# Kernel tuning notes

Hardware: AMD Instinct MI355X
Metric: run time of the kernel (lower is better)

The kernel has to match this reference:

```python
import jax, jax.numpy as jnp
import numpy as np
from jax import lax

NUM_TAGS = 126
T = NUM_TAGS + 2          # tag_size = 128
B, S = 256, 512
START, STOP = T - 3, T - 2
NEG = -10000.0


def setup_inputs() -> dict:
    key = jax.random.key(0)
    k1, k2, k3 = jax.random.split(key, 3)
    feats = jax.random.normal(k1, (B, S, T), jnp.float32)
    # learned transition matrix with the module's init masking pattern
    trans = jax.random.normal(k2, (T, T), jnp.float32)
    trans = trans.at[:, START].set(NEG).at[STOP, :].set(NEG)
    trans = trans.at[:, 0].set(NEG).at[0, :].set(NEG)
    # prefix masks with varying valid lengths in [S/2, S]
    lengths = jax.random.randint(k3, (B,), S // 2, S + 1)
    mask = jnp.arange(S)[None, :] < lengths[:, None]
    return {"feats": feats, "mask": mask, "transitions": trans}


def reference(feats, mask, transitions):
    # Viterbi decode (module.forward returns (None, decode_idx)).
    Bn, Sn, Tn = feats.shape
    start, stop = Tn - 3, Tn - 2
    emit = jnp.transpose(feats, (1, 0, 2))            # (S, B, T)
    m = jnp.transpose(mask.astype(jnp.int32))         # (S, B)
    lengths = mask.astype(jnp.int32).sum(axis=1)      # (B,)

    part0 = emit[0] + transitions[start][None, :]     # (B, T)

    def step(part, inp):
        e_t, m_t = inp
        # scores[t, b, i, j] = feats[t, b, j] + transitions[i, j]
        cur = part[:, :, None] + transitions[None, :, :] + e_t[:, None, :]  # (B, from, to)
        new_part = cur.max(axis=1)                                          # (B, T)
        bp = jnp.argmax(cur, axis=1).astype(jnp.int32)                      # (B, T)
        bp = jnp.where(m_t[:, None] > 0, bp, 0)
        return new_part, (new_part, bp)

    _, (hist, bps) = lax.scan(step, part0, (emit[1:], m[1:]))
    part_hist = jnp.concatenate([part0[None], hist], axis=0)                # (S, B, T)
    back_points = jnp.concatenate(
        [bps, jnp.zeros((1, Bn, Tn), jnp.int32)], axis=0)                   # (S, B, T)

    bidx = jnp.arange(Bn)
    last_pos = lengths - 1                                                  # (B,)
    last_partition = part_hist[last_pos, bidx]                              # (B, T)
    last_bp = jnp.argmax(last_partition[:, :, None] + transitions[None], axis=1)
    pointer = last_bp[:, stop].astype(jnp.int32)                            # (B,)

    # overwrite back_points at the last valid position with the final pointer
    bp_bt = jnp.transpose(back_points, (1, 0, 2))                           # (B, S, T)
    bp_bt = bp_bt.at[bidx, last_pos].set(
        jnp.broadcast_to(pointer[:, None], (Bn, Tn)))
    back_points = jnp.transpose(bp_bt, (1, 0, 2))                           # (S, B, T)

    def trace(ptr, bp_t):
        new_ptr = jnp.take_along_axis(bp_t, ptr[:, None], axis=1)[:, 0]
        return new_ptr, new_ptr

    _, rev = lax.scan(trace, pointer, back_points[:-1], reverse=True)       # (S-1, B)
    decode = jnp.concatenate([rev, pointer[None]], axis=0)                  # (S, B)
    return jnp.transpose(decode)                                            # (B, S)
```

## Files before the change

### kernel.cpp

```cpp
#include <hip/hip_runtime.h>
#include <cstdint>
#include <cstddef>

constexpr int T_ = 128;
constexpr int S_ = 512;
constexpr int B_ = 256;
constexpr int START_ = T_ - 3;
constexpr int STOP_  = T_ - 2;
constexpr float NEGINF_ = -3.402823466e38f;

__global__ __launch_bounds__(256) void viterbi_forward(
    const float* __restrict__ feats,
    const float* __restrict__ trans,
    float* __restrict__ ph)
{
  const int b   = blockIdx.x;
  const int tid = threadIdx.x;
  const int j   = tid & (T_ - 1);
  const int h   = tid >> 7;

  __shared__ alignas(16) float part[T_];
  __shared__ float partial[2][T_];

  float tc[64];
  #pragma unroll
  for (int ii = 0; ii < 64; ++ii)
    tc[ii] = trans[(h * 64 + ii) * T_ + j];

  const float* fb = feats + (size_t)b * S_ * T_;

  float p0 = fb[j] + trans[START_ * T_ + j];
  if (h == 0) {
    part[j] = p0;
    ph[(size_t)b * T_ + j] = p0;
  }
  float e_next = fb[T_ + j];
  __syncthreads();

  for (int t = 1; t < S_; ++t) {
    float e_cur = e_next;
    if (t + 1 < S_) e_next = fb[(size_t)(t + 1) * T_ + j];

    const float4* p4 = (const float4*)part;
    float ma = NEGINF_, mb = NEGINF_;
    #pragma unroll
    for (int q = 0; q < 16; q += 2) {
      float4 pa = p4[h * 16 + q];
      float a0 = pa.x + tc[4 * q + 0];
      float a1 = pa.y + tc[4 * q + 1];
      float a2 = pa.z + tc[4 * q + 2];
      float a3 = pa.w + tc[4 * q + 3];
      ma = fmaxf(ma, fmaxf(fmaxf(a0, a1), fmaxf(a2, a3)));
      float4 pb = p4[h * 16 + q + 1];
      float b0 = pb.x + tc[4 * q + 4];
      float b1 = pb.y + tc[4 * q + 5];
      float b2 = pb.z + tc[4 * q + 6];
      float b3 = pb.w + tc[4 * q + 7];
      mb = fmaxf(mb, fmaxf(fmaxf(b0, b1), fmaxf(b2, b3)));
    }
    partial[h][j] = fmaxf(ma, mb);
    __syncthreads();
    if (h == 0) {
      float np = fmaxf(partial[0][j], partial[1][j]) + e_cur;
      part[j] = np;
      ph[((size_t)t * B_ + b) * T_ + j] = np;
    }
    __syncthreads();
  }
}

constexpr int CH_ = 8;

__global__ __launch_bounds__(64) void viterbi_trace(
    const float* __restrict__ feats,
    const void*  __restrict__ mask,
    const float* __restrict__ trans,
    const float* __restrict__ ph,
    int* __restrict__ out)
{
  const int b    = blockIdx.x;
  const int lane = threadIdx.x;

  __shared__ float transT[T_ * 129];

  #pragma unroll 4
  for (int g = lane; g < T_ * T_; g += 64) {
    int i  = g >> 7;
    int jj = g & (T_ - 1);
    transT[jj * 129 + i] = trans[g];
  }
  __syncthreads();

  int len = 0;
  {
    const int w0 = *(const int*)mask;
    if (w0 == 0x01010101) {
      const unsigned char* m = (const unsigned char*)mask + (size_t)b * S_;
      for (int s = lane; s < S_; s += 64) len += (m[s] != 0);
    } else if (w0 == 0x3F800000) {
      const float* m = (const float*)mask + (size_t)b * S_;
      for (int s = lane; s < S_; s += 64) len += (m[s] != 0.0f);
    } else {
      const int* m = (const int*)mask + (size_t)b * S_;
      for (int s = lane; s < S_; s += 64) len += (m[s] != 0);
    }
    #pragma unroll
    for (int o = 32; o > 0; o >>= 1) len += __shfl_xor(len, o);
  }
  const int lp = len - 1;

  const float* lastrow = ph + ((size_t)lp * B_ + b) * T_;
  float v0 = lastrow[lane]      + transT[STOP_ * 129 + lane];
  float v1 = lastrow[lane + 64] + transT[STOP_ * 129 + 64 + lane];
  float mx = fmaxf(v0, v1);
  #pragma unroll
  for (int o = 32; o > 0; o >>= 1) mx = fmaxf(mx, __shfl_xor(mx, o));
  unsigned long long g0 = __ballot(v0 == mx);
  unsigned long long g1 = __ballot(v1 == mx);
  int pointer = g0 ? (__ffsll(g0) - 1) : (64 + __ffsll(g1) - 1);

  int ptr = pointer;
  if (lane == 0) out[b * S_ + (S_ - 1)] = pointer;

  const float* fb = feats + (size_t)b * S_ * T_;

  float Aph[CH_][2], Apn[CH_][2], Afe[CH_][2];
  float Bph[CH_][2], Bpn[CH_][2], Bfe[CH_][2];

  auto issue = [&](float (&P)[CH_][2], float (&N)[CH_][2], float (&F)[CH_][2],
                   int k0) {
    #pragma unroll
    for (int s = 0; s < CH_; ++s) {
      int k = k0 - s;
      if (k < 0) k = 0;
      const float* rp = ph + ((size_t)k       * B_ + b) * T_;
      const float* rn = ph + ((size_t)(k + 1) * B_ + b) * T_;
      const float* rf = fb + (size_t)(k + 1) * T_;
      P[s][0] = rp[lane];      P[s][1] = rp[lane + 64];
      N[s][0] = rn[lane];      N[s][1] = rn[lane + 64];
      F[s][0] = rf[lane];      F[s][1] = rf[lane + 64];
    }
  };

  auto process = [&](float (&P)[CH_][2], float (&N)[CH_][2], float (&F)[CH_][2],
                     int k0) {
    #pragma unroll
    for (int s = 0; s < CH_; ++s) {
      const int kk = k0 - s;
      if (kk >= 0) {
        int val;
        if (kk > lp) {
          val = 0;
        } else if (kk == lp) {
          ptr = pointer;
          val = pointer;
        } else {
          float tr0 = transT[ptr * 129 + lane];
          float tr1 = transT[ptr * 129 + 64 + lane];
          const int pl = ptr & 63;
          float e  = __shfl((ptr < 64) ? F[s][0] : F[s][1], pl);
          float tg = __shfl((ptr < 64) ? N[s][0] : N[s][1], pl);
          float c0 = (P[s][0] + tr0) + e;
          float c1 = (P[s][1] + tr1) + e;
          unsigned long long m0 = __ballot(c0 == tg);
          unsigned long long m1 = __ballot(c1 == tg);
          ptr = m0 ? (__ffsll(m0) - 1) : (64 + __ffsll(m1) - 1);
          val = ptr;
        }
        if (lane == 0) out[b * S_ + kk] = val;
      }
    }
  };

  issue(Aph, Apn, Afe, S_ - 2);
  for (int k0 = S_ - 2; k0 >= 0; k0 -= 2 * CH_) {
    issue(Bph, Bpn, Bfe, k0 - CH_);
    process(Aph, Apn, Afe, k0);
    issue(Aph, Apn, Afe, k0 - 2 * CH_);
    process(Bph, Bpn, Bfe, k0 - CH_);
  }
}

extern "C" void kernel_launch(void* const* d_in, const int* in_sizes, int n_in,
                              void* d_out, int out_size, void* d_ws, size_t ws_size,
                              hipStream_t stream) {
  const float* feats = (const float*)d_in[0];
  const void*  mask  = d_in[1];
  const float* trans = (const float*)d_in[2];
  float* ph = (float*)d_ws;
  int*   out = (int*)d_out;

  viterbi_forward<<<dim3(B_), dim3(256), 0, stream>>>(feats, trans, ph);
  viterbi_trace  <<<dim3(B_), dim3(64),  0, stream>>>(feats, mask, trans, ph, out);
}
```

Measured before the change: 473.9 us.

## Use shuffle reduction and double-buffered LDS in forward; batch chains in traceback

In the forward kernel the two halves of each column now sit in adjacent lanes, so the partial maxima are combined with a shuffle instead of a shared-memory round trip. The partition vector is double-buffered, which removes one of the two barriers per step, and the barrier becomes a raw waitcnt plus s_barrier. The traceback kernel now interleaves four batch chains per wave, reusing the previous step's partition row as the target value and keeping a rolling prefetch window of depth four. The aim is shorter per-step latency on both serial recurrences, at the cost of a quarter as many trace blocks and more register pressure.

```diff
diff --git a/kernel.cpp b/kernel.cpp
--- a/kernel.cpp
+++ b/kernel.cpp
@@ -9,6 +9,10 @@
 constexpr int STOP_  = T_ - 2;
 constexpr float NEGINF_ = -3.402823466e38f;
 
+__device__ __forceinline__ void lds_barrier() {
+  asm volatile("s_waitcnt lgkmcnt(0)\n\ts_barrier" ::: "memory");
+}
+
 __global__ __launch_bounds__(256) void viterbi_forward(
     const float* __restrict__ feats,
     const float* __restrict__ trans,
@@ -16,11 +20,10 @@
 {
   const int b   = blockIdx.x;
   const int tid = threadIdx.x;
-  const int j   = tid & (T_ - 1);
-  const int h   = tid >> 7;
+  const int j   = tid >> 1;
+  const int h   = tid & 1;
 
-  __shared__ alignas(16) float part[T_];
-  __shared__ float partial[2][T_];
+  __shared__ alignas(16) float part[2][T_];
 
   float tc[64];
   #pragma unroll
@@ -31,7 +34,7 @@
 
   float p0 = fb[j] + trans[START_ * T_ + j];
   if (h == 0) {
-    part[j] = p0;
+    part[0][j] = p0;
     ph[(size_t)b * T_ + j] = p0;
   }
   float e_next = fb[T_ + j];
@@ -41,35 +44,35 @@
     float e_cur = e_next;
     if (t + 1 < S_) e_next = fb[(size_t)(t + 1) * T_ + j];
 
-    const float4* p4 = (const float4*)part;
-    float ma = NEGINF_, mb = NEGINF_;
+    const float4* p4 = (const float4*)part[(t - 1) & 1];
+    float m0 = NEGINF_, m1 = NEGINF_, m2 = NEGINF_, m3 = NEGINF_;
     #pragma unroll
-    for (int q = 0; q < 16; q += 2) {
-      float4 pa = p4[h * 16 + q];
-      float a0 = pa.x + tc[4 * q + 0];
-      float a1 = pa.y + tc[4 * q + 1];
-      float a2 = pa.z + tc[4 * q + 2];
-      float a3 = pa.w + tc[4 * q + 3];
-      ma = fmaxf(ma, fmaxf(fmaxf(a0, a1), fmaxf(a2, a3)));
-      float4 pb = p4[h * 16 + q + 1];
-      float b0 = pb.x + tc[4 * q + 4];
-      float b1 = pb.y + tc[4 * q + 5];
-      float b2 = pb.z + tc[4 * q + 6];
-      float b3 = pb.w + tc[4 * q + 7];
-      mb = fmaxf(mb, fmaxf(fmaxf(b0, b1), fmaxf(b2, b3)));
+    for (int q = 0; q < 16; q += 4) {
+      float4 a0 = p4[h * 16 + q + 0];
+      float4 a1 = p4[h * 16 + q + 1];
+      float4 a2 = p4[h * 16 + q + 2];
+      float4 a3 = p4[h * 16 + q + 3];
+      m0 = fmaxf(m0, fmaxf(fmaxf(a0.x + tc[4*q+ 0], a0.y + tc[4*q+ 1]),
+                           fmaxf(a0.z + tc[4*q+ 2], a0.w + tc[4*q+ 3])));
+      m1 = fmaxf(m1, fmaxf(fmaxf(a1.x + tc[4*q+ 4], a1.y + tc[4*q+ 5]),
+                           fmaxf(a1.z + tc[4*q+ 6], a1.w + tc[4*q+ 7])));
+      m2 = fmaxf(m2, fmaxf(fmaxf(a2.x + tc[4*q+ 8], a2.y + tc[4*q+ 9]),
+                           fmaxf(a2.z + tc[4*q+10], a2.w + tc[4*q+11])));
+      m3 = fmaxf(m3, fmaxf(fmaxf(a3.x + tc[4*q+12], a3.y + tc[4*q+13]),
+                           fmaxf(a3.z + tc[4*q+14], a3.w + tc[4*q+15])));
     }
-    partial[h][j] = fmaxf(ma, mb);
-    __syncthreads();
-    if (h == 0) {
-      float np = fmaxf(partial[0][j], partial[1][j]) + e_cur;
-      part[j] = np;
-      ph[((size_t)t * B_ + b) * T_ + j] = np;
-    }
-    __syncthreads();
+    float m = fmaxf(fmaxf(m0, m1), fmaxf(m2, m3));
+    m = fmaxf(m, __shfl_xor(m, 1));
+    float np = m + e_cur;
+    if (h == 0) part[t & 1][j] = np;
+    lds_barrier();
+    if (h == 0) ph[((size_t)t * B_ + b) * T_ + j] = np;
   }
 }
 
-constexpr int CH_ = 8;
+constexpr int NC_ = 4;
+constexpr int D_  = 4;
+constexpr int TS_ = 130;
 
 __global__ __launch_bounds__(64) void viterbi_trace(
     const float* __restrict__ feats,
@@ -78,22 +81,27 @@
     const float* __restrict__ ph,
     int* __restrict__ out)
 {
-  const int b    = blockIdx.x;
   const int lane = threadIdx.x;
+  const int b0   = blockIdx.x * NC_;
 
-  __shared__ float transT[T_ * 129];
-
+  __shared__ alignas(16) float transT[T_ * TS_];
   #pragma unroll 4
   for (int g = lane; g < T_ * T_; g += 64) {
-    int i  = g >> 7;
-    int jj = g & (T_ - 1);
-    transT[jj * 129 + i] = trans[g];
+    int i = g >> 7, jj = g & (T_ - 1);
+    transT[jj * TS_ + i] = trans[g];
   }
   __syncthreads();
 
-  int len = 0;
-  {
-    const int w0 = *(const int*)mask;
+  const int w0 = *(const int*)mask;
+
+  int    lp[NC_], ptrc[NC_], pointer[NC_];
+  float  tg[NC_], e[NC_];
+  float2 P[NC_][D_], F[NC_][D_];
+
+  #pragma unroll
+  for (int c = 0; c < NC_; ++c) {
+    const int b = b0 + c;
+    int len = 0;
     if (w0 == 0x01010101) {
       const unsigned char* m = (const unsigned char*)mask + (size_t)b * S_;
       for (int s = lane; s < S_; s += 64) len += (m[s] != 0);
@@ -106,78 +114,68 @@
     }
     #pragma unroll
     for (int o = 32; o > 0; o >>= 1) len += __shfl_xor(len, o);
+    lp[c] = len - 1;
+
+    float2 L = ((const float2*)(ph + ((size_t)lp[c] * B_ + b) * T_))[lane];
+    float v0 = L.x + transT[STOP_ * TS_ + 2 * lane];
+    float v1 = L.y + transT[STOP_ * TS_ + 2 * lane + 1];
+    float mx = fmaxf(v0, v1);
+    #pragma unroll
+    for (int o = 32; o > 0; o >>= 1) mx = fmaxf(mx, __shfl_xor(mx, o));
+    unsigned long long m0 = __ballot(v0 == mx);
+    unsigned long long m1 = __ballot(v1 == mx);
+    int p0 = m0 ? 2 * (__ffsll(m0) - 1)     : (1 << 30);
+    int p1 = m1 ? 2 * (__ffsll(m1) - 1) + 1 : (1 << 30);
+    int p  = min(p0, p1);
+    pointer[c] = p;
+    ptrc[c]    = p;
+    if (lane == 0) out[b * S_ + (S_ - 1)] = p;
+
+    tg[c] = __shfl((p & 1) ? L.y : L.x, p >> 1);
+    float2 FL = ((const float2*)(feats + ((size_t)b * S_ + lp[c]) * T_))[lane];
+    e[c] = __shfl((p & 1) ? FL.y : FL.x, p >> 1);
+
+    #pragma unroll
+    for (int d = 0; d < D_; ++d) {
+      int kr = S_ - 2 - d; if (kr < 0) kr = 0;
+      P[c][d] = ((const float2*)(ph    + ((size_t)kr * B_ + b) * T_))[lane];
+      F[c][d] = ((const float2*)(feats + ((size_t)b * S_ + kr) * T_))[lane];
+    }
   }
-  const int lp = len - 1;
 
-  const float* lastrow = ph + ((size_t)lp * B_ + b) * T_;
-  float v0 = lastrow[lane]      + transT[STOP_ * 129 + lane];
-  float v1 = lastrow[lane + 64] + transT[STOP_ * 129 + 64 + lane];
-  float mx = fmaxf(v0, v1);
-  #pragma unroll
-  for (int o = 32; o > 0; o >>= 1) mx = fmaxf(mx, __shfl_xor(mx, o));
-  unsigned long long g0 = __ballot(v0 == mx);
-  unsigned long long g1 = __ballot(v1 == mx);
-  int pointer = g0 ? (__ffsll(g0) - 1) : (64 + __ffsll(g1) - 1);
+  for (int k = S_ - 2; k >= 0; --k) {
+    #pragma unroll
+    for (int c = 0; c < NC_; ++c) {
+      const int b = b0 + c;
+      int val;
+      if (k > lp[c]) {
+        val = 0;
+      } else if (k == lp[c]) {
+        ptrc[c] = pointer[c];
+        val = pointer[c];
+      } else {
+        const float* tr = transT + ptrc[c] * TS_ + 2 * lane;
+        float cx = (P[c][0].x + tr[0]) + e[c];
+        float cy = (P[c][0].y + tr[1]) + e[c];
+        unsigned long long q0 = __ballot(cx == tg[c]);
+        unsigned long long q1 = __ballot(cy == tg[c]);
+        int a0 = q0 ? 2 * (__ffsll(q0) - 1)     : (1 << 30);
+        int a1 = q1 ? 2 * (__ffsll(q1) - 1) + 1 : (1 << 30);
+        ptrc[c] = min(a0, a1);
+        val = ptrc[c];
+      }
+      if (lane == 0) out[b * S_ + k] = val;
 
-  int ptr = pointer;
-  if (lane == 0) out[b * S_ + (S_ - 1)] = pointer;
+      int p = ptrc[c], pl = p >> 1;
+      tg[c] = __shfl((p & 1) ? P[c][0].y : P[c][0].x, pl);
+      e[c]  = __shfl((p & 1) ? F[c][0].y : F[c][0].x, pl);
 
-  const float* fb = feats + (size_t)b * S_ * T_;
-
-  float Aph[CH_][2], Apn[CH_][2], Afe[CH_][2];
-  float Bph[CH_][2], Bpn[CH_][2], Bfe[CH_][2];
-
-  auto issue = [&](float (&P)[CH_][2], float (&N)[CH_][2], float (&F)[CH_][2],
-                   int k0) {
-    #pragma unroll
-    for (int s = 0; s < CH_; ++s) {
-      int k = k0 - s;
-      if (k < 0) k = 0;
-      const float* rp = ph + ((size_t)k       * B_ + b) * T_;
-      const float* rn = ph + ((size_t)(k + 1) * B_ + b) * T_;
-      const float* rf = fb + (size_t)(k + 1) * T_;
-      P[s][0] = rp[lane];      P[s][1] = rp[lane + 64];
-      N[s][0] = rn[lane];      N[s][1] = rn[lane + 64];
-      F[s][0] = rf[lane];      F[s][1] = rf[lane + 64];
+      #pragma unroll
+      for (int d = 0; d < D_ - 1; ++d) { P[c][d] = P[c][d + 1]; F[c][d] = F[c][d + 1]; }
+      int kr = k - D_; if (kr < 0) kr = 0;
+      P[c][D_ - 1] = ((const float2*)(ph    + ((size_t)kr * B_ + b) * T_))[lane];
+      F[c][D_ - 1] = ((const float2*)(feats + ((size_t)b * S_ + kr) * T_))[lane];
     }
-  };
-
-  auto process = [&](float (&P)[CH_][2], float (&N)[CH_][2], float (&F)[CH_][2],
-                     int k0) {
-    #pragma unroll
-    for (int s = 0; s < CH_; ++s) {
-      const int kk = k0 - s;
-      if (kk >= 0) {
-        int val;
-        if (kk > lp) {
-          val = 0;
-        } else if (kk == lp) {
-          ptr = pointer;
-          val = pointer;
-        } else {
-          float tr0 = transT[ptr * 129 + lane];
-          float tr1 = transT[ptr * 129 + 64 + lane];
-          const int pl = ptr & 63;
-          float e  = __shfl((ptr < 64) ? F[s][0] : F[s][1], pl);
-          float tg = __shfl((ptr < 64) ? N[s][0] : N[s][1], pl);
-          float c0 = (P[s][0] + tr0) + e;
-          float c1 = (P[s][1] + tr1) + e;
-          unsigned long long m0 = __ballot(c0 == tg);
-          unsigned long long m1 = __ballot(c1 == tg);
-          ptr = m0 ? (__ffsll(m0) - 1) : (64 + __ffsll(m1) - 1);
-          val = ptr;
-        }
-        if (lane == 0) out[b * S_ + kk] = val;
-      }
-    }
-  };
-
-  issue(Aph, Apn, Afe, S_ - 2);
-  for (int k0 = S_ - 2; k0 >= 0; k0 -= 2 * CH_) {
-    issue(Bph, Bpn, Bfe, k0 - CH_);
-    process(Aph, Apn, Afe, k0);
-    issue(Aph, Apn, Afe, k0 - 2 * CH_);
-    process(Bph, Bpn, Bfe, k0 - CH_);
   }
 }
 
@@ -191,5 +189,5 @@
   int*   out = (int*)d_out;
 
   viterbi_forward<<<dim3(B_), dim3(256), 0, stream>>>(feats, trans, ph);
-  viterbi_trace  <<<dim3(B_), dim3(64),  0, stream>>>(feats, mask, trans, ph, out);
+  viterbi_trace  <<<dim3(B_ / NC_), dim3(64), 0, stream>>>(feats, mask, trans, ph, out);
 }
```

Result: slower. 908.5 us (+91.7%).
